# Optimization experiments

Measured on AMD Instinct MI355X. Metric: run time of the kernel, lower is better.

Reference implementation:

```python
import jax, jax.numpy as jnp
import numpy as np

B, T, IN, H, OUT = 2048, 4096, 1, 8, 1


def setup_inputs() -> dict:
    key = jax.random.key(0)
    ks = jax.random.split(key, 11)
    s_in = 1.0 / np.sqrt(H)  # torch nn.LSTM/Linear init scale (uniform +-1/sqrt(H))
    u = lambda k, shape, s: jax.random.uniform(k, shape, jnp.float32, -s, s)
    return {
        "input_seq": jax.random.normal(ks[0], (B, T, IN), jnp.float32),
        # layer 0 (input_size=IN)
        "W_ih0": u(ks[1], (4 * H, IN), s_in),
        "W_hh0": u(ks[2], (4 * H, H), s_in),
        "b_ih0": u(ks[3], (4 * H,), s_in),
        "b_hh0": u(ks[4], (4 * H,), s_in),
        # layer 1 (input_size=H)
        "W_ih1": u(ks[5], (4 * H, H), s_in),
        "W_hh1": u(ks[6], (4 * H, H), s_in),
        "b_ih1": u(ks[7], (4 * H,), s_in),
        "b_hh1": u(ks[8], (4 * H,), s_in),
        # output projection
        "W_lin": u(ks[9], (OUT, H), s_in),
        "b_lin": u(ks[10], (OUT,), s_in),
    }


def _lstm_layer(x_tbi, W_ih, W_hh, b_ih, b_hh):
    """x_tbi: [T, B, in] -> hidden sequence [T, B, H]. PyTorch gate order i,f,g,o."""
    h_dim = W_hh.shape[1]
    # precompute input contribution for all timesteps (hoisted out of the scan)
    xg = jnp.einsum('tbi,gi->tbg', x_tbi, W_ih) + (b_ih + b_hh)  # [T, B, 4H]
    bsz = x_tbi.shape[1]
    h0 = jnp.zeros((bsz, h_dim), x_tbi.dtype)
    c0 = jnp.zeros((bsz, h_dim), x_tbi.dtype)

    def step(carry, xg_t):
        h, c = carry
        gates = xg_t + h @ W_hh.T  # [B, 4H]
        i, f, g, o = jnp.split(gates, 4, axis=-1)
        i = jax.nn.sigmoid(i)
        f = jax.nn.sigmoid(f)
        g = jnp.tanh(g)
        o = jax.nn.sigmoid(o)
        c = f * c + i * g
        h = o * jnp.tanh(c)
        return (h, c), h

    _, hs = jax.lax.scan(step, (h0, c0), xg)
    return hs  # [T, B, H]


def reference(input_seq, W_ih0, W_hh0, b_ih0, b_hh0,
              W_ih1, W_hh1, b_ih1, b_hh1, W_lin, b_lin):
    x = jnp.transpose(input_seq, (1, 0, 2))  # [T, B, IN] (batch_first -> time-major)
    h1 = _lstm_layer(x, W_ih0, W_hh0, b_ih0, b_hh0)   # [T, B, H]
    h2 = _lstm_layer(h1, W_ih1, W_hh1, b_ih1, b_hh1)  # [T, B, H]
    out = jnp.transpose(h2, (1, 0, 2))                # [B, T, H]
    pred = out @ W_lin.T + b_lin                      # [B, T, OUT]
    return pred
```

## Files before the change

### kernel.cpp

```cpp
#include <hip/hip_runtime.h>


constexpr int Bsz = 2048;
constexpr int Tsz = 4096;

typedef float v2f __attribute__((ext_vector_type(2)));

__device__ __forceinline__ void pk_fma(v2f& acc, v2f a, v2f b) {
    asm("v_pk_fma_f32 %0, %1, %2, %0" : "+v"(acc) : "v"(a), "v"(b));
}

template <int CTRL>
__device__ __forceinline__ float dpp(float v) {
    return __int_as_float(
        __builtin_amdgcn_mov_dpp(__float_as_int(v), CTRL, 0xF, 0xF, true));
}

template <int XORM>
__device__ __forceinline__ float swz(float v) {
    return __int_as_float(
        __builtin_amdgcn_ds_swizzle(__float_as_int(v), (XORM << 10) | 0x1f));
}

__device__ __forceinline__ float bperm(int addr, float v) {
    return __int_as_float(
        __builtin_amdgcn_ds_bpermute(addr, __float_as_int(v)));
}

__global__ void __launch_bounds__(256, 2) lstm2_q64(
    const float* __restrict__ x,
    const float* __restrict__ Wih0,
    const float* __restrict__ Whh0,
    const float* __restrict__ bih0,
    const float* __restrict__ bhh0,
    const float* __restrict__ Wih1,
    const float* __restrict__ Whh1,
    const float* __restrict__ bih1,
    const float* __restrict__ bhh1,
    const float* __restrict__ Wlin,
    const float* __restrict__ blin,
    float* __restrict__ out)
{
    const int tid  = threadIdx.x;
    const int lane = tid & 63;
    const int g    = lane & 3;
    const int j    = (lane >> 2) & 7;
    const int L    = (lane >> 5) & 1;
    const int seq  = blockIdx.x * 4 + (tid >> 6);

    const int r = g * 8 + j;

    const float NL2E  = -1.4426950408889634f;
    const float N2L2E = -2.8853900817779268f;
    const bool  isG   = (g == 2);
    const float ws    = isG ? N2L2E : NL2E;
    const float sA    = isG ? 2.0f : 1.0f;
    const float oA    = isG ? -1.0f : 0.0f;

    const float* __restrict__ Whh = L ? Whh1 : Whh0;
    const float* __restrict__ bih = L ? bih1 : bih0;
    const float* __restrict__ bhh = L ? bhh1 : bhh0;

    v2f wp1[4], wp2[4];
#pragma unroll
    for (int q = 0; q < 4; ++q) {
        const int kx = j ^ (2 * q);
        const int ky = j ^ (2 * q + 1);
        wp1[q] = v2f{Whh[r * 8 + kx] * ws, Whh[r * 8 + ky] * ws};
        wp2[q] = L ? v2f{Wlin[kx], Wlin[ky]}
                   : v2f{Wih1[r * 8 + kx] * ws, Wih1[r * 8 + ky] * ws};
    }
    const float bias = (bih[r] + bhh[r]) * ws;
    const float wx   = L ? 0.0f : Wih0[r] * ws;
    const float b2   = L ? blin[0] : 0.0f;
    const float mL   = L ? 1.0f : 0.0f;
    const float keep = 1.0f - mL;
    const int  xaddr = (lane ^ 32) * 4;

    const float* __restrict__ xp = x + (size_t)seq * Tsz;
    float* __restrict__ op       = out + (size_t)seq * Tsz;
    const bool storeLane = (lane == 32);

    v2f hp[4];
#pragma unroll
    for (int q = 0; q < 4; ++q) hp[q] = v2f{0.0f, 0.0f};
    float c = 0.0f, h = 0.0f, recv = 0.0f;

    float xn1 = xp[0];
    float xn2 = xp[1];

    auto body = [&](int t) {
        const float xt = xn1;
        xn1 = xn2;
        int ti = t + 2; ti = (ti < Tsz) ? ti : (Tsz - 1);
        xn2 = xp[ti];

        v2f a1 = v2f{fmaf(wx, xt, bias), 0.0f};
        v2f a2 = v2f{b2, 0.0f};
#pragma unroll
        for (int q = 0; q < 4; ++q) {
            pk_fma(a1, wp1[q], hp[q]);
            pk_fma(a2, wp2[q], hp[q]);
        }
        const float d1 = a1.x + a1.y;
        const float d2 = a2.x + a2.y;

        if (t >= 3 && storeLane) op[t - 3] = d2;

        const float rOld = recv;
        recv = bperm(xaddr, d2);

        const float z = fmaf(mL, rOld, d1);
        float a = fmaf(sA,
                       __builtin_amdgcn_rcpf(1.0f + __builtin_amdgcn_exp2f(z)),
                       oA);
        const float gi = dpp<0x00>(a);
        const float gf = dpp<0x55>(a);
        const float gG = dpp<0xAA>(a);
        const float go = dpp<0xFF>(a);
        c = fmaf(gf, c, gi * gG);
        const float e  = __builtin_amdgcn_exp2f(c * N2L2E);
        const float th = fmaf(2.0f, __builtin_amdgcn_rcpf(1.0f + e), -1.0f);
        h = go * th;

        const float m7  = dpp<0x141>(h);
        const float h1_ = dpp<0x1B>(m7);
        const float m15 = dpp<0x140>(h);
        const float h2_ = dpp<0x141>(m15);
        const float h3_ = dpp<0x1B>(m15);
        const float h4_ = swz<16>(h);
        const float h5_ = swz<20>(h);
        const float h6_ = swz<24>(h);
        const float h7_ = swz<28>(h);
        hp[0] = v2f{h,   h1_};
        hp[1] = v2f{h2_, h3_};
        hp[2] = v2f{h4_, h5_};
        hp[3] = v2f{h6_, h7_};
    };

    body(0);
    h *= keep; c *= keep;
#pragma unroll
    for (int q = 0; q < 4; ++q) { hp[q].x *= keep; hp[q].y *= keep; }
    body(1);
    h *= keep; c *= keep;
#pragma unroll
    for (int q = 0; q < 4; ++q) { hp[q].x *= keep; hp[q].y *= keep; }

    for (int t = 2; t <= Tsz + 2; ++t) body(t);
}

extern "C" void kernel_launch(void* const* d_in, const int* in_sizes, int n_in,
                              void* d_out, int out_size, void* d_ws, size_t ws_size,
                              hipStream_t stream) {
    const float* x    = (const float*)d_in[0];
    const float* Wih0 = (const float*)d_in[1];
    const float* Whh0 = (const float*)d_in[2];
    const float* bih0 = (const float*)d_in[3];
    const float* bhh0 = (const float*)d_in[4];
    const float* Wih1 = (const float*)d_in[5];
    const float* Whh1 = (const float*)d_in[6];
    const float* bih1 = (const float*)d_in[7];
    const float* bhh1 = (const float*)d_in[8];
    const float* Wlin = (const float*)d_in[9];
    const float* blin = (const float*)d_in[10];
    float* out = (float*)d_out;

    dim3 grid(Bsz / 4);
    dim3 block(256);
    hipLaunchKernelGGL(lstm2_q64, grid, block, 0, stream,
                       x, Wih0, Whh0, bih0, bhh0,
                       Wih1, Whh1, bih1, bhh1, Wlin, blin, out);
}
```

Before: 948.5 us.

## Split hidden-state dot product across lane halves to cut swizzles per step

Each lane now computes partial dot products for its own row and its partner row (j^4) over only 4 hidden elements, then exchanges the partner half with one ds_swizzle instead of broadcasting 4 extra hidden values via four swizzles. Packed FMAs are replaced by scalar FMAs, the layer pipeline is deepened to a two-step bperm delay, and the time loop is unrolled by 4 with batched x prefetch. This aims to shorten the serial per-timestep latency chain dominated by cross-lane data movement, at the cost of more scalar FMA instructions and a longer pipeline fill.

```diff
diff --git a/kernel.cpp b/kernel.cpp
--- a/kernel.cpp
+++ b/kernel.cpp
@@ -3,12 +3,6 @@
 
 constexpr int Bsz = 2048;
 constexpr int Tsz = 4096;
-
-typedef float v2f __attribute__((ext_vector_type(2)));
-
-__device__ __forceinline__ void pk_fma(v2f& acc, v2f a, v2f b) {
-    asm("v_pk_fma_f32 %0, %1, %2, %0" : "+v"(acc) : "v"(a), "v"(b));
-}
 
 template <int CTRL>
 __device__ __forceinline__ float dpp(float v) {
@@ -16,18 +10,16 @@
         __builtin_amdgcn_mov_dpp(__float_as_int(v), CTRL, 0xF, 0xF, true));
 }
 
-template <int XORM>
-__device__ __forceinline__ float swz(float v) {
+__device__ __forceinline__ float swz16(float v) {
     return __int_as_float(
-        __builtin_amdgcn_ds_swizzle(__float_as_int(v), (XORM << 10) | 0x1f));
+        __builtin_amdgcn_ds_swizzle(__float_as_int(v), (16 << 10) | 0x1f));
 }
 
 __device__ __forceinline__ float bperm(int addr, float v) {
-    return __int_as_float(
-        __builtin_amdgcn_ds_bpermute(addr, __float_as_int(v)));
+    return __int_as_float(__builtin_amdgcn_ds_bpermute(addr, __float_as_int(v)));
 }
 
-__global__ void __launch_bounds__(256, 2) lstm2_q64(
+__global__ void __launch_bounds__(256, 2) lstm2_mp2(
     const float* __restrict__ x,
     const float* __restrict__ Wih0,
     const float* __restrict__ Whh0,
@@ -48,7 +40,9 @@
     const int L    = (lane >> 5) & 1;
     const int seq  = blockIdx.x * 4 + (tid >> 6);
 
-    const int r = g * 8 + j;
+    const int jm = j ^ 4;
+    const int r  = g * 8 + j;
+    const int rm = g * 8 + jm;
 
     const float NL2E  = -1.4426950408889634f;
     const float N2L2E = -2.8853900817779268f;
@@ -61,14 +55,14 @@
     const float* __restrict__ bih = L ? bih1 : bih0;
     const float* __restrict__ bhh = L ? bhh1 : bhh0;
 
-    v2f wp1[4], wp2[4];
+    float wn1[4], wm1[4], wn2[4], wm2[4];
 #pragma unroll
-    for (int q = 0; q < 4; ++q) {
-        const int kx = j ^ (2 * q);
-        const int ky = j ^ (2 * q + 1);
-        wp1[q] = v2f{Whh[r * 8 + kx] * ws, Whh[r * 8 + ky] * ws};
-        wp2[q] = L ? v2f{Wlin[kx], Wlin[ky]}
-                   : v2f{Wih1[r * 8 + kx] * ws, Wih1[r * 8 + ky] * ws};
+    for (int i = 0; i < 4; ++i) {
+        const int k = j ^ i;
+        wn1[i] = Whh[r * 8 + k] * ws;
+        wm1[i] = Whh[rm * 8 + k] * ws;
+        wn2[i] = L ? Wlin[k] : Wih1[r * 8 + k] * ws;
+        wm2[i] = L ? Wlin[k] : Wih1[rm * 8 + k] * ws;
     }
     const float bias = (bih[r] + bhh[r]) * ws;
     const float wx   = L ? 0.0f : Wih0[r] * ws;
@@ -81,36 +75,34 @@
     float* __restrict__ op       = out + (size_t)seq * Tsz;
     const bool storeLane = (lane == 32);
 
-    v2f hp[4];
-#pragma unroll
-    for (int q = 0; q < 4; ++q) hp[q] = v2f{0.0f, 0.0f};
-    float c = 0.0f, h = 0.0f, recv = 0.0f;
+    float hn0 = 0.0f, hn1 = 0.0f, hn2 = 0.0f, hn3 = 0.0f;
+    float c = 0.0f, h = 0.0f;
+    float recvA = 0.0f, recvB = 0.0f;
 
-    float xn1 = xp[0];
-    float xn2 = xp[1];
+    auto body = [&](float xt, bool fill, float* storePtr) {
+        float am1 = wm1[0] * hn0;
+        am1 = fmaf(wm1[1], hn1, am1);
+        am1 = fmaf(wm1[2], hn2, am1);
+        am1 = fmaf(wm1[3], hn3, am1);
+        float am2 = wm2[0] * hn0;
+        am2 = fmaf(wm2[1], hn1, am2);
+        am2 = fmaf(wm2[2], hn2, am2);
+        am2 = fmaf(wm2[3], hn3, am2);
+        const float s1 = swz16(am1);
+        const float s2 = swz16(am2);
 
-    auto body = [&](int t) {
-        const float xt = xn1;
-        xn1 = xn2;
-        int ti = t + 2; ti = (ti < Tsz) ? ti : (Tsz - 1);
-        xn2 = xp[ti];
+        float an1 = fmaf(wx, xt, bias);
+        an1 = fmaf(wn1[0], hn0, an1);
+        an1 = fmaf(wn1[1], hn1, an1);
+        an1 = fmaf(wn1[2], hn2, an1);
+        an1 = fmaf(wn1[3], hn3, an1);
+        float an2 = fmaf(wn2[0], hn0, b2);
+        an2 = fmaf(wn2[1], hn1, an2);
+        an2 = fmaf(wn2[2], hn2, an2);
+        an2 = fmaf(wn2[3], hn3, an2);
 
-        v2f a1 = v2f{fmaf(wx, xt, bias), 0.0f};
-        v2f a2 = v2f{b2, 0.0f};
-#pragma unroll
-        for (int q = 0; q < 4; ++q) {
-            pk_fma(a1, wp1[q], hp[q]);
-            pk_fma(a2, wp2[q], hp[q]);
-        }
-        const float d1 = a1.x + a1.y;
-        const float d2 = a2.x + a2.y;
+        const float z = fmaf(mL, recvB, an1 + s1);
 
-        if (t >= 3 && storeLane) op[t - 3] = d2;
-
-        const float rOld = recv;
-        recv = bperm(xaddr, d2);
-
-        const float z = fmaf(mL, rOld, d1);
         float a = fmaf(sA,
                        __builtin_amdgcn_rcpf(1.0f + __builtin_amdgcn_exp2f(z)),
                        oA);
@@ -123,31 +115,44 @@
         const float th = fmaf(2.0f, __builtin_amdgcn_rcpf(1.0f + e), -1.0f);
         h = go * th;
 
+        if (fill) { h *= keep; c *= keep; }
+
         const float m7  = dpp<0x141>(h);
-        const float h1_ = dpp<0x1B>(m7);
         const float m15 = dpp<0x140>(h);
-        const float h2_ = dpp<0x141>(m15);
-        const float h3_ = dpp<0x1B>(m15);
-        const float h4_ = swz<16>(h);
-        const float h5_ = swz<20>(h);
-        const float h6_ = swz<24>(h);
-        const float h7_ = swz<28>(h);
-        hp[0] = v2f{h,   h1_};
-        hp[1] = v2f{h2_, h3_};
-        hp[2] = v2f{h4_, h5_};
-        hp[3] = v2f{h6_, h7_};
+        hn0 = h;
+        hn1 = dpp<0x1B>(m7);
+        hn2 = dpp<0x141>(m15);
+        hn3 = dpp<0x1B>(m15);
+
+        const float d2 = an2 + s2;
+        if (storePtr && storeLane) *storePtr = d2;
+        recvB = recvA;
+        recvA = bperm(xaddr, d2);
     };
 
-    body(0);
-    h *= keep; c *= keep;
+    body(xp[0], true, nullptr);
+    body(xp[1], true, nullptr);
+    body(xp[2], true, nullptr);
+    body(xp[3], false, nullptr);
+
+    float xc[4];
 #pragma unroll
-    for (int q = 0; q < 4; ++q) { hp[q].x *= keep; hp[q].y *= keep; }
-    body(1);
-    h *= keep; c *= keep;
+    for (int u = 0; u < 4; ++u) xc[u] = xp[4 + u];
+    for (int ck = 0; ck < Tsz / 4; ++ck) {
+        const int base = 4 + 4 * ck;
+        float xf[4];
 #pragma unroll
-    for (int q = 0; q < 4; ++q) { hp[q].x *= keep; hp[q].y *= keep; }
-
-    for (int t = 2; t <= Tsz + 2; ++t) body(t);
+        for (int u = 0; u < 4; ++u) {
+            int idx = base + 4 + u;
+            idx = (idx < Tsz) ? idx : (Tsz - 1);
+            xf[u] = xp[idx];
+        }
+#pragma unroll
+        for (int u = 0; u < 4; ++u)
+            body(xc[u], false, op + (4 * ck + u));
+#pragma unroll
+        for (int u = 0; u < 4; ++u) xc[u] = xf[u];
+    }
 }
 
 extern "C" void kernel_launch(void* const* d_in, const int* in_sizes, int n_in,
@@ -168,7 +173,7 @@
 
     dim3 grid(Bsz / 4);
     dim3 block(256);
-    hipLaunchKernelGGL(lstm2_q64, grid, block, 0, stream,
+    hipLaunchKernelGGL(lstm2_mp2, grid, block, 0, stream,
                        x, Wih0, Whh0, bih0, bhh0,
                        Wih1, Whh1, bih1, bhh1, Wlin, blin, out);
 }
```

Result: faster. 896.9 us (-5.4%).
